# Performance work log

Measured on AMD Instinct MI355X. Metric: run time of the kernel, lower is better.

The kernel has to match this reference:

```python
import math
import jax, jax.numpy as jnp
import numpy as np

FACTOR = 5

def setup_inputs() -> dict:
    key = jax.random.key(0)
    k1, k2, k3, k4 = jax.random.split(key, 4)
    B, L, H, E = 4, 2048, 8, 64
    sample_k = min(L, max(1, int(FACTOR * math.ceil(math.log(L + 1)))))  # 40
    return {
        "queries": jax.random.normal(k1, (B, L, H, E), jnp.float32),
        "keys": jax.random.normal(k2, (B, L, H, E), jnp.float32),
        "values": jax.random.normal(k3, (B, L, H, E), jnp.float32),
        "index_sample": jax.random.randint(k4, (L, sample_k), 0, L),
    }

def reference(queries, keys, values, index_sample):
    # queries/keys/values: [B, L, H, E]; index_sample: [Lq, sample_k] int
    B, Lq, H, E = queries.shape
    Lk = keys.shape[1]
    q = jnp.transpose(queries, (0, 2, 1, 3))  # [B,H,Lq,E]
    k = jnp.transpose(keys, (0, 2, 1, 3))     # [B,H,Lk,E]
    v = jnp.transpose(values, (0, 2, 1, 3))   # [B,H,Lk,E]

    n_top = min(Lq, max(1, int(FACTOR * math.ceil(math.log(Lq + 1)))))
    scale = 1.0 / math.sqrt(E)

    # --- ProbSparse query scoring: sample keys per query, measure sparsity ---
    k_sample = k[:, :, index_sample, :]                       # [B,H,Lq,sk,E]
    qk_sample = jnp.einsum('bhle,bhlse->bhls', q, k_sample)   # [B,H,Lq,sk]
    sparsity = qk_sample.max(axis=-1) - qk_sample.mean(axis=-1)  # [B,H,Lq]
    _, top_idx = jax.lax.top_k(sparsity, n_top)               # [B,H,n_top]

    # --- Full scores only for the top queries ---
    q_top = jnp.take_along_axis(q, top_idx[..., None], axis=2)    # [B,H,n_top,E]
    scores = jnp.einsum('bhne,bhke->bhnk', q_top, k) * scale      # [B,H,n_top,Lk]

    # causal mask on the gathered rows (mask_flag=True, attn_mask=None)
    key_pos = jnp.arange(Lk)
    mask = key_pos[None, None, None, :] > top_idx[..., None]
    scores = jnp.where(mask, -jnp.inf, scores)
    attn = jax.nn.softmax(scores, axis=-1)                        # dropout = identity (eval)
    updates = jnp.einsum('bhnk,bhke->bhne', attn, v)              # [B,H,n_top,E]

    # --- cumsum-initialized context, scatter sparse rows back ---
    context = jnp.cumsum(v, axis=2)                               # [B,H,Lq,E]
    bi = jnp.arange(B)[:, None, None]
    hi = jnp.arange(H)[None, :, None]
    context = context.at[bi, hi, top_idx].set(updates)
    return jnp.transpose(context, (0, 2, 1, 3))                   # [B,Lq,H,E]
```

## Files before the change

### kernel.cpp

```cpp
#include <hip/hip_runtime.h>
#include <hip/hip_bf16.h>

#define BB 4
#define LL 2048
#define HH 8
#define EE 64
#define SK 40
#define NT 40
#define BH (BB*HH)
#define NCH 128
#define CLEN (LL/NCH)
#define KS 128
#define NS (LL/KS)

__device__ __forceinline__ size_t ro(int b, int l, int h) {
    return ((size_t)(b*LL + l)*HH + h)*EE;
}
__device__ __forceinline__ float bcast(float x, int sl) {
    return __uint_as_float(__builtin_amdgcn_readlane(__float_as_uint(x), sl));
}

__global__ __launch_bounds__(256) void k_spars(const float* __restrict__ q,
                                               const float* __restrict__ k,
                                               const int* __restrict__ samp,
                                               float* __restrict__ spars)
{
    __shared__ float pbuf[4][SK][20];
    int wid  = (blockIdx.x * blockDim.x + threadIdx.x) >> 6;
    int lane = threadIdx.x & 63;
    int w    = threadIdx.x >> 6;
    int bh = wid / LL;
    int l  = wid - bh * LL;
    int b = bh >> 3, h = bh & 7;

    int sidx = (lane < SK) ? samp[l*SK + lane] : 0;

    const float4* qrow = (const float4*)(q + ro(b, l, h));
    float4 q4 = qrow[lane & 15];

    int sub = lane >> 4;
    #pragma unroll
    for (int g = 0; g < SK/4; ++g) {
        int s = 4*g + sub;
        int row = __shfl(sidx, s, 64);
        const float4* kr = (const float4*)(k + ro(b, row, h));
        float4 k4 = kr[lane & 15];
        float p = k4.x*q4.x + k4.y*q4.y + k4.z*q4.z + k4.w*q4.w;
        pbuf[w][s][lane & 15] = p;
    }
    float dot = 0.f;
    if (lane < SK) {
        const float4* pr = (const float4*)&pbuf[w][lane][0];
        float4 a = pr[0], b4 = pr[1], c4 = pr[2], d4 = pr[3];
        dot = ((a.x+a.y)+(a.z+a.w)) + ((b4.x+b4.y)+(b4.z+b4.w))
            + ((c4.x+c4.y)+(c4.z+c4.w)) + ((d4.x+d4.y)+(d4.z+d4.w));
    }
    float dmax = (lane < SK) ? dot : -INFINITY;
    float dsum = (lane < SK) ? dot : 0.f;
    #pragma unroll
    for (int off = 32; off; off >>= 1) {
        dmax = fmaxf(dmax, __shfl_xor(dmax, off, 64));
        dsum += __shfl_xor(dsum, off, 64);
    }
    if (lane == 0) spars[bh*LL + l] = dmax - dsum * (1.0f/SK);
}

__global__ __launch_bounds__(256) void k_topk(const float* __restrict__ spars,
                                              int* __restrict__ topidx,
                                              int* __restrict__ sel)
{
    __shared__ float wv[4];
    __shared__ int   wi[4];
    __shared__ int   top[NT];
    int bh = blockIdx.x, t = threadIdx.x, w = t >> 6, lane = t & 63;

    float r[8];
    #pragma unroll
    for (int i = 0; i < 8; ++i) r[i] = spars[bh*LL + i*256 + t];

    for (int n = 0; n < NT; ++n) {
        float bv = r[0]; int bi = t;
        #pragma unroll
        for (int i = 1; i < 8; ++i)
            if (r[i] > bv) { bv = r[i]; bi = i*256 + t; }
        #pragma unroll
        for (int off = 32; off; off >>= 1) {
            float ov = __shfl_xor(bv, off, 64);
            int   oi = __shfl_xor(bi, off, 64);
            if (ov > bv || (ov == bv && oi < bi)) { bv = ov; bi = oi; }
        }
        if (lane == 0) { wv[w] = bv; wi[w] = bi; }
        __syncthreads();
        float gv = wv[0]; int gi = wi[0];
        #pragma unroll
        for (int j = 1; j < 4; ++j) {
            float ov = wv[j]; int oi = wi[j];
            if (ov > gv || (ov == gv && oi < gi)) { gv = ov; gi = oi; }
        }
        if (t == 0) { top[n] = gi; topidx[bh*NT + n] = gi; }
        if ((gi & 255) == t) {
            int slot = gi >> 8;
            #pragma unroll
            for (int i = 0; i < 8; ++i) if (i == slot) r[i] = -INFINITY;
        }
        __syncthreads();
    }

    for (int l2 = t; l2 < LL; l2 += 256) sel[bh*LL + l2] = -1;
    __syncthreads();
    if (t < NT) sel[bh*LL + top[t]] = t;
}

__global__ __launch_bounds__(256) void k_attn_split(const float* __restrict__ q,
                                                    const float* __restrict__ k,
                                                    const float* __restrict__ v,
                                                    const int* __restrict__ topidx,
                                                    float* __restrict__ pm,
                                                    float* __restrict__ pl,
                                                    float* __restrict__ pO)
{
    __shared__ float KT[EE][KS+1];
    __shared__ float Vs[KS][EE];
    __shared__ float Qs[NT][EE];
    __shared__ int   tix[NT];
    __shared__ int   maxti_s;
    int bh = blockIdx.x / NS, split = blockIdx.x % NS;
    int b = bh >> 3, h = bh & 7;
    int base = split * KS;
    int t = threadIdx.x, w = t >> 6, lane = t & 63;

    if (t < NT) tix[t] = topidx[bh*NT + t];
    __syncthreads();
    if (t == 0) { int m = 0; for (int i = 0; i < NT; ++i) m = max(m, tix[i]); maxti_s = m; }
    __syncthreads();
    int jmaxAll = min(KS, maxti_s - base + 1);

    int rr = t >> 4, c4 = t & 15;
    for (int p = 0; p < 3; ++p) {
        int n = p*16 + rr;
        if (n < NT) {
            const float4* qr = (const float4*)(q + ro(b, tix[n], h));
            float4 x = qr[c4];
            Qs[n][c4*4+0] = x.x*0.125f; Qs[n][c4*4+1] = x.y*0.125f;
            Qs[n][c4*4+2] = x.z*0.125f; Qs[n][c4*4+3] = x.w*0.125f;
        }
    }
    for (int p = 0; p < KS/16; ++p) {
        int kr = p*16 + rr;
        if (kr < jmaxAll) {
            const float4* krow = (const float4*)(k + ro(b, base + kr, h));
            float4 x = krow[c4];
            KT[c4*4+0][kr] = x.x; KT[c4*4+1][kr] = x.y;
            KT[c4*4+2][kr] = x.z; KT[c4*4+3][kr] = x.w;
            const float4* vrow = (const float4*)(v + ro(b, base + kr, h));
            ((float4*)&Vs[kr][0])[c4] = vrow[c4];
        }
    }
    __syncthreads();

    for (int jj = 0; jj < 5; ++jj) {
        int na = w + 8*jj, nb = w + 8*jj + 4;
        int ja = min(KS, tix[na] - base + 1);
        int jb = min(KS, tix[nb] - base + 1);
        bool aa = ja > 0, ab = jb > 0;
        size_t pba = ((size_t)(bh*NT + na)*NS + split);
        size_t pbb = ((size_t)(bh*NT + nb)*NS + split);
        int jp = max(ja, jb);
        if (jp <= 0) {
            if (lane == 0) { pm[pba] = -INFINITY; pl[pba] = 0.f; pm[pbb] = -INFINITY; pl[pbb] = 0.f; }
            pO[pba*EE + lane] = 0.f;
            pO[pbb*EE + lane] = 0.f;
            continue;
        }
        float s0a = 0, s1a = 0, s0b = 0, s1b = 0;
        #pragma unroll 4
        for (int e = 0; e < EE; ++e) {
            float k0 = KT[e][lane], k1 = KT[e][64+lane];
            float qa = Qs[na][e],  qb = Qs[nb][e];
            s0a += qa*k0; s1a += qa*k1;
            s0b += qb*k0; s1b += qb*k1;
        }
        s0a = (lane      < ja) ? s0a : -INFINITY;
        s1a = (lane + 64 < ja) ? s1a : -INFINITY;
        s0b = (lane      < jb) ? s0b : -INFINITY;
        s1b = (lane + 64 < jb) ? s1b : -INFINITY;
        float ma = fmaxf(s0a, s1a), mb = fmaxf(s0b, s1b);
        #pragma unroll
        for (int off = 32; off; off >>= 1) {
            ma = fmaxf(ma, __shfl_xor(ma, off, 64));
            mb = fmaxf(mb, __shfl_xor(mb, off, 64));
        }
        float p0a = aa ? __expf(s0a - ma) : 0.f;
        float p1a = aa ? __expf(s1a - ma) : 0.f;
        float p0b = ab ? __expf(s0b - mb) : 0.f;
        float p1b = ab ? __expf(s1b - mb) : 0.f;
        float la = p0a + p1a, lb = p0b + p1b;
        #pragma unroll
        for (int off = 32; off; off >>= 1) {
            la += __shfl_xor(la, off, 64);
            lb += __shfl_xor(lb, off, 64);
        }
        float oa = 0.f, ob = 0.f;
        int lim0 = min(64, jp);
        #pragma unroll 4
        for (int kk = 0; kk < lim0; ++kk) {
            float vv = Vs[kk][lane];
            oa += bcast(p0a, kk) * vv;
            ob += bcast(p0b, kk) * vv;
        }
        int lim1 = min(64, jp - 64);
        #pragma unroll 4
        for (int kk = 0; kk < lim1; ++kk) {
            float vv = Vs[64+kk][lane];
            oa += bcast(p1a, kk) * vv;
            ob += bcast(p1b, kk) * vv;
        }
        if (lane == 0) {
            pm[pba] = aa ? ma : -INFINITY;  pl[pba] = aa ? la : 0.f;
            pm[pbb] = ab ? mb : -INFINITY;  pl[pbb] = ab ? lb : 0.f;
        }
        pO[pba*EE + lane] = aa ? oa : 0.f;
        pO[pbb*EE + lane] = ab ? ob : 0.f;
    }
}

__global__ __launch_bounds__(256) void k_attn_comb(const float* __restrict__ pm,
                                                   const float* __restrict__ pl,
                                                   const float* __restrict__ pO,
                                                   float* __restrict__ upd)
{
    int wid  = (blockIdx.x * blockDim.x + threadIdx.x) >> 6;
    int lane = threadIdx.x & 63;
    if (wid >= BH*NT) return;
    float M = -INFINITY;
    #pragma unroll
    for (int s = 0; s < NS; ++s) M = fmaxf(M, pm[wid*NS + s]);
    float L = 0.f, O = 0.f;
    #pragma unroll
    for (int s = 0; s < NS; ++s) {
        float ms = pm[wid*NS + s];
        float sc = __expf(ms - M);
        L += pl[wid*NS + s] * sc;
        O += pO[(size_t)(wid*NS + s)*EE + lane] * sc;
    }
    upd[(size_t)wid*EE + lane] = O / L;
}

__global__ __launch_bounds__(256) void k_attn_old(const float* __restrict__ q,
                                                  const float* __restrict__ k,
                                                  const float* __restrict__ v,
                                                  const int* __restrict__ topidx,
                                                  float* __restrict__ upd)
{
    __shared__ float sc[LL];
    __shared__ float red[256];
    __shared__ float part[4][EE];
    int bh = blockIdx.x / NT, n = blockIdx.x % NT;
    int b = bh >> 3, h = bh & 7;
    int ti = topidx[bh*NT + n];
    int t = threadIdx.x, w = t >> 6, lane = t & 63;

    float qe = q[ro(b, ti, h) + lane];
    for (int j = w; j <= ti; j += 4) {
        float kv = k[ro(b, j, h) + lane];
        float p = qe * kv;
        #pragma unroll
        for (int off = 32; off; off >>= 1) p += __shfl_xor(p, off, 64);
        if (lane == 0) sc[j] = p * 0.125f;
    }
    __syncthreads();
    float m = -1e30f;
    for (int j = t; j <= ti; j += 256) m = fmaxf(m, sc[j]);
    red[t] = m; __syncthreads();
    for (int s2 = 128; s2; s2 >>= 1) { if (t < s2) red[t] = fmaxf(red[t], red[t+s2]); __syncthreads(); }
    m = red[0]; __syncthreads();
    float ssum = 0.f;
    for (int j = t; j <= ti; j += 256) { float p = __expf(sc[j] - m); sc[j] = p; ssum += p; }
    red[t] = ssum; __syncthreads();
    for (int s2 = 128; s2; s2 >>= 1) { if (t < s2) red[t] += red[t+s2]; __syncthreads(); }
    float inv = 1.0f / red[0];
    float acc = 0.f;
    for (int j = w; j <= ti; j += 4) acc += sc[j] * v[ro(b, j, h) + lane];
    part[w][lane] = acc;
    __syncthreads();
    if (w == 0) {
        float r = (part[0][lane] + part[1][lane] + part[2][lane] + part[3][lane]) * inv;
        upd[((size_t)bh*NT + n)*EE + lane] = r;
    }
}

__global__ __launch_bounds__(256) void k_csum(const float* __restrict__ v,
                                              float* __restrict__ csum)
{
    int wid  = (blockIdx.x * blockDim.x + threadIdx.x) >> 6;
    int lane = threadIdx.x & 63;
    int bh = wid / NCH, c = wid - bh*NCH;
    int b = bh >> 3, h = bh & 7;
    int l0 = c * CLEN;
    float s = 0.f;
    #pragma unroll 4
    for (int i = 0; i < CLEN; ++i)
        s += v[ro(b, l0 + i, h) + lane];
    csum[(size_t)wid*EE + lane] = s;
}

__global__ __launch_bounds__(256) void k_pfx(float* __restrict__ csum)
{
    int wid  = (blockIdx.x * blockDim.x + threadIdx.x) >> 6;
    int lane = threadIdx.x & 63;
    if (wid >= BH) return;
    float run = 0.f;
    for (int c = 0; c < NCH; ++c) {
        size_t a = ((size_t)wid*NCH + c)*EE + lane;
        float x = csum[a];
        csum[a] = run;
        run += x;
    }
}

__global__ __launch_bounds__(256) void k_out(const float* __restrict__ v,
                                             const float* __restrict__ csum,
                                             const int* __restrict__ sel,
                                             const float* __restrict__ upd,
                                             float* __restrict__ out)
{
    int wid  = (blockIdx.x * blockDim.x + threadIdx.x) >> 6;
    int lane = threadIdx.x & 63;
    int bh = wid / NCH, c = wid - bh*NCH;
    int b = bh >> 3, h = bh & 7;

    float run = csum[((size_t)bh*NCH + c)*EE + lane];
    int l0 = c * CLEN;
    #pragma unroll 4
    for (int i = 0; i < CLEN; ++i) {
        int l = l0 + i;
        run += v[ro(b, l, h) + lane];
        int sn = sel[bh*LL + l];
        float val = (sn >= 0) ? upd[((size_t)bh*NT + sn)*EE + lane] : run;
        out[ro(b, l, h) + lane] = val;
    }
}

extern "C" void kernel_launch(void* const* d_in, const int* in_sizes, int n_in,
                              void* d_out, int out_size, void* d_ws, size_t ws_size,
                              hipStream_t stream) {
    const float* q = (const float*)d_in[0];
    const float* k = (const float*)d_in[1];
    const float* v = (const float*)d_in[2];
    const int* samp = (const int*)d_in[3];
    float* out = (float*)d_out;

    char* ws = (char*)d_ws;
    size_t o = 0;
    float* spars  = (float*)(ws + o); o += (size_t)BH*LL*4;
    int*   topidx = (int*)  (ws + o); o += 8192;
    int*   sel    = (int*)  (ws + o); o += (size_t)BH*LL*4;
    float* upd    = (float*)(ws + o); o += (size_t)BH*NT*EE*4;
    float* csum   = (float*)(ws + o); o += (size_t)BH*NCH*EE*4;
    size_t base_need = o;
    float* pm = (float*)(ws + o); o += (size_t)BH*NT*NS*4;
    float* pl = (float*)(ws + o); o += (size_t)BH*NT*NS*4;
    float* pO = (float*)(ws + o); o += (size_t)BH*NT*NS*EE*4;
    size_t full_need = o;

    k_spars<<<BH*LL/4, 256, 0, stream>>>(q, k, samp, spars);
    k_topk <<<BH,      256, 0, stream>>>(spars, topidx, sel);
    if (ws_size >= full_need) {
        k_attn_split<<<BH*NS, 256, 0, stream>>>(q, k, v, topidx, pm, pl, pO);
        k_attn_comb <<<BH*NT/4, 256, 0, stream>>>(pm, pl, pO, upd);
    } else if (ws_size >= base_need) {
        k_attn_old<<<BH*NT, 256, 0, stream>>>(q, k, v, topidx, upd);
    }
    k_csum<<<BH*NCH/4, 256, 0, stream>>>(v, csum);
    k_pfx <<<(BH+3)/4, 256, 0, stream>>>(csum);
    k_out <<<BH*NCH/4, 256, 0, stream>>>(v, csum, sel, upd, out);
}
```

Baseline: 225.2 us.

## Restructure split attention with register-blocked queries, bf16 partials, parallel prefix

Halves the key split size and makes each wave keep 10 query rows in registers, broadcasting q and probabilities via readlane instead of staging Q in LDS. The causal early-skip of key loads is dropped. Partial outputs are stored as bf16, and the combine step reduces split maxima with wave shuffles. The selection map shrinks to int8, the prefix scan becomes a per-head LDS-blocked kernel, k_spars blocks are remapped so neighbouring blocks cover different heads, and workspace buffers are aliased. The bf16 partials add rounding error to the sparse updates.

```diff
diff --git a/kernel.cpp b/kernel.cpp
--- a/kernel.cpp
+++ b/kernel.cpp
@@ -10,8 +10,9 @@
 #define BH (BB*HH)
 #define NCH 128
 #define CLEN (LL/NCH)
-#define KS 128
+#define KS 64
 #define NS (LL/KS)
+#define NQW 10
 
 __device__ __forceinline__ size_t ro(int b, int l, int h) {
     return ((size_t)(b*LL + l)*HH + h)*EE;
@@ -26,11 +27,11 @@
                                                float* __restrict__ spars)
 {
     __shared__ float pbuf[4][SK][20];
-    int wid  = (blockIdx.x * blockDim.x + threadIdx.x) >> 6;
+    int bid = blockIdx.x;
+    int w    = threadIdx.x >> 6;
     int lane = threadIdx.x & 63;
-    int w    = threadIdx.x >> 6;
-    int bh = wid / LL;
-    int l  = wid - bh * LL;
+    int bh = (((bid >> 3) & 3) << 3) | (bid & 7);
+    int l  = (bid >> 5) * 4 + w;
     int b = bh >> 3, h = bh & 7;
 
     int sidx = (lane < SK) ? samp[l*SK + lane] : 0;
@@ -67,7 +68,7 @@
 
 __global__ __launch_bounds__(256) void k_topk(const float* __restrict__ spars,
                                               int* __restrict__ topidx,
-                                              int* __restrict__ sel)
+                                              signed char* __restrict__ sel)
 {
     __shared__ float wv[4];
     __shared__ int   wi[4];
@@ -108,7 +109,7 @@
 
     for (int l2 = t; l2 < LL; l2 += 256) sel[bh*LL + l2] = -1;
     __syncthreads();
-    if (t < NT) sel[bh*LL + top[t]] = t;
+    if (t < NT) sel[bh*LL + top[t]] = (signed char)t;
 }
 
 __global__ __launch_bounds__(256) void k_attn_split(const float* __restrict__ q,
@@ -117,133 +118,179 @@
                                                     const int* __restrict__ topidx,
                                                     float* __restrict__ pm,
                                                     float* __restrict__ pl,
-                                                    float* __restrict__ pO)
+                                                    __hip_bfloat16* __restrict__ pO)
 {
     __shared__ float KT[EE][KS+1];
     __shared__ float Vs[KS][EE];
-    __shared__ float Qs[NT][EE];
     __shared__ int   tix[NT];
-    __shared__ int   maxti_s;
-    int bh = blockIdx.x / NS, split = blockIdx.x % NS;
+    int bh = blockIdx.x >> 5, split = blockIdx.x & 31;
     int b = bh >> 3, h = bh & 7;
     int base = split * KS;
     int t = threadIdx.x, w = t >> 6, lane = t & 63;
 
     if (t < NT) tix[t] = topidx[bh*NT + t];
     __syncthreads();
-    if (t == 0) { int m = 0; for (int i = 0; i < NT; ++i) m = max(m, tix[i]); maxti_s = m; }
-    __syncthreads();
-    int jmaxAll = min(KS, maxti_s - base + 1);
 
     int rr = t >> 4, c4 = t & 15;
-    for (int p = 0; p < 3; ++p) {
-        int n = p*16 + rr;
-        if (n < NT) {
-            const float4* qr = (const float4*)(q + ro(b, tix[n], h));
-            float4 x = qr[c4];
-            Qs[n][c4*4+0] = x.x*0.125f; Qs[n][c4*4+1] = x.y*0.125f;
-            Qs[n][c4*4+2] = x.z*0.125f; Qs[n][c4*4+3] = x.w*0.125f;
-        }
-    }
-    for (int p = 0; p < KS/16; ++p) {
+    #pragma unroll
+    for (int p = 0; p < 4; ++p) {
         int kr = p*16 + rr;
-        if (kr < jmaxAll) {
-            const float4* krow = (const float4*)(k + ro(b, base + kr, h));
-            float4 x = krow[c4];
-            KT[c4*4+0][kr] = x.x; KT[c4*4+1][kr] = x.y;
-            KT[c4*4+2][kr] = x.z; KT[c4*4+3][kr] = x.w;
-            const float4* vrow = (const float4*)(v + ro(b, base + kr, h));
-            ((float4*)&Vs[kr][0])[c4] = vrow[c4];
-        }
-    }
-    __syncthreads();
-
-    for (int jj = 0; jj < 5; ++jj) {
-        int na = w + 8*jj, nb = w + 8*jj + 4;
-        int ja = min(KS, tix[na] - base + 1);
-        int jb = min(KS, tix[nb] - base + 1);
-        bool aa = ja > 0, ab = jb > 0;
-        size_t pba = ((size_t)(bh*NT + na)*NS + split);
-        size_t pbb = ((size_t)(bh*NT + nb)*NS + split);
-        int jp = max(ja, jb);
-        if (jp <= 0) {
-            if (lane == 0) { pm[pba] = -INFINITY; pl[pba] = 0.f; pm[pbb] = -INFINITY; pl[pbb] = 0.f; }
-            pO[pba*EE + lane] = 0.f;
-            pO[pbb*EE + lane] = 0.f;
-            continue;
-        }
-        float s0a = 0, s1a = 0, s0b = 0, s1b = 0;
-        #pragma unroll 4
-        for (int e = 0; e < EE; ++e) {
-            float k0 = KT[e][lane], k1 = KT[e][64+lane];
-            float qa = Qs[na][e],  qb = Qs[nb][e];
-            s0a += qa*k0; s1a += qa*k1;
-            s0b += qb*k0; s1b += qb*k1;
-        }
-        s0a = (lane      < ja) ? s0a : -INFINITY;
-        s1a = (lane + 64 < ja) ? s1a : -INFINITY;
-        s0b = (lane      < jb) ? s0b : -INFINITY;
-        s1b = (lane + 64 < jb) ? s1b : -INFINITY;
-        float ma = fmaxf(s0a, s1a), mb = fmaxf(s0b, s1b);
-        #pragma unroll
-        for (int off = 32; off; off >>= 1) {
-            ma = fmaxf(ma, __shfl_xor(ma, off, 64));
-            mb = fmaxf(mb, __shfl_xor(mb, off, 64));
-        }
-        float p0a = aa ? __expf(s0a - ma) : 0.f;
-        float p1a = aa ? __expf(s1a - ma) : 0.f;
-        float p0b = ab ? __expf(s0b - mb) : 0.f;
-        float p1b = ab ? __expf(s1b - mb) : 0.f;
-        float la = p0a + p1a, lb = p0b + p1b;
-        #pragma unroll
-        for (int off = 32; off; off >>= 1) {
-            la += __shfl_xor(la, off, 64);
-            lb += __shfl_xor(lb, off, 64);
-        }
-        float oa = 0.f, ob = 0.f;
-        int lim0 = min(64, jp);
-        #pragma unroll 4
-        for (int kk = 0; kk < lim0; ++kk) {
-            float vv = Vs[kk][lane];
-            oa += bcast(p0a, kk) * vv;
-            ob += bcast(p0b, kk) * vv;
-        }
-        int lim1 = min(64, jp - 64);
-        #pragma unroll 4
-        for (int kk = 0; kk < lim1; ++kk) {
-            float vv = Vs[64+kk][lane];
-            oa += bcast(p1a, kk) * vv;
-            ob += bcast(p1b, kk) * vv;
-        }
-        if (lane == 0) {
-            pm[pba] = aa ? ma : -INFINITY;  pl[pba] = aa ? la : 0.f;
-            pm[pbb] = ab ? mb : -INFINITY;  pl[pbb] = ab ? lb : 0.f;
-        }
-        pO[pba*EE + lane] = aa ? oa : 0.f;
-        pO[pbb*EE + lane] = ab ? ob : 0.f;
+        const float4* krow = (const float4*)(k + ro(b, base + kr, h));
+        float4 x = krow[c4];
+        KT[c4*4+0][kr] = x.x; KT[c4*4+1][kr] = x.y;
+        KT[c4*4+2][kr] = x.z; KT[c4*4+3][kr] = x.w;
+        const float4* vrow = (const float4*)(v + ro(b, base + kr, h));
+        ((float4*)&Vs[kr][0])[c4] = vrow[c4];
+    }
+
+    float qreg[NQW]; int jn[NQW];
+    #pragma unroll
+    for (int r = 0; r < NQW; ++r) {
+        int ti = tix[w*NQW + r];
+        jn[r] = min(KS, ti - base + 1);
+        qreg[r] = q[ro(b, ti, h) + lane] * 0.125f;
+    }
+    __syncthreads();
+
+    float S[NQW];
+    #pragma unroll
+    for (int r = 0; r < NQW; ++r) S[r] = 0.f;
+    for (int e0 = 0; e0 < EE; e0 += 16) {
+        #pragma unroll
+        for (int j = 0; j < 16; ++j) {
+            int e = e0 + j;
+            float ke = KT[e][lane];
+            #pragma unroll
+            for (int r = 0; r < NQW; ++r)
+                S[r] = fmaf(ke, bcast(qreg[r], e), S[r]);
+        }
+    }
+
+    float P[NQW], mloc[NQW], lloc[NQW];
+    #pragma unroll
+    for (int r = 0; r < NQW; ++r) {
+        float s = (lane < jn[r]) ? S[r] : -INFINITY;
+        float m = s;
+        #pragma unroll
+        for (int off = 32; off; off >>= 1) m = fmaxf(m, __shfl_xor(m, off, 64));
+        bool act = jn[r] > 0;
+        float p = act ? __expf(s - m) : 0.f;
+        float ls = p;
+        #pragma unroll
+        for (int off = 32; off; off >>= 1) ls += __shfl_xor(ls, off, 64);
+        P[r] = p; mloc[r] = act ? m : -INFINITY; lloc[r] = act ? ls : 0.f;
+    }
+
+    float O[NQW];
+    #pragma unroll
+    for (int r = 0; r < NQW; ++r) O[r] = 0.f;
+    for (int k0 = 0; k0 < KS; k0 += 16) {
+        #pragma unroll
+        for (int j = 0; j < 16; ++j) {
+            int kk = k0 + j;
+            float ve = Vs[kk][lane];
+            #pragma unroll
+            for (int r = 0; r < NQW; ++r)
+                O[r] = fmaf(ve, bcast(P[r], kk), O[r]);
+        }
+    }
+
+    #pragma unroll
+    for (int r = 0; r < NQW; ++r) {
+        int n = w*NQW + r;
+        size_t idx = (size_t)(bh*NT + n)*NS + split;
+        if (lane == 0) { pm[idx] = mloc[r]; pl[idx] = lloc[r]; }
+        pO[idx*EE + lane] = __float2bfloat16(O[r]);
     }
 }
 
 __global__ __launch_bounds__(256) void k_attn_comb(const float* __restrict__ pm,
                                                    const float* __restrict__ pl,
-                                                   const float* __restrict__ pO,
+                                                   const __hip_bfloat16* __restrict__ pO,
                                                    float* __restrict__ upd)
 {
     int wid  = (blockIdx.x * blockDim.x + threadIdx.x) >> 6;
     int lane = threadIdx.x & 63;
-    if (wid >= BH*NT) return;
-    float M = -INFINITY;
-    #pragma unroll
-    for (int s = 0; s < NS; ++s) M = fmaxf(M, pm[wid*NS + s]);
-    float L = 0.f, O = 0.f;
-    #pragma unroll
+    float pmv = (lane < NS) ? pm[(size_t)wid*NS + lane] : -INFINITY;
+    float plv = (lane < NS) ? pl[(size_t)wid*NS + lane] : 0.f;
+    float M = pmv;
+    #pragma unroll
+    for (int off = 32; off; off >>= 1) M = fmaxf(M, __shfl_xor(M, off, 64));
+    float sc = (lane < NS && pmv > -INFINITY) ? __expf(pmv - M) : 0.f;
+    float L = plv * sc;
+    #pragma unroll
+    for (int off = 32; off; off >>= 1) L += __shfl_xor(L, off, 64);
+    float O = 0.f;
     for (int s = 0; s < NS; ++s) {
-        float ms = pm[wid*NS + s];
-        float sc = __expf(ms - M);
-        L += pl[wid*NS + s] * sc;
-        O += pO[(size_t)(wid*NS + s)*EE + lane] * sc;
+        float w = bcast(sc, s);
+        O += __bfloat162float(pO[((size_t)wid*NS + s)*EE + lane]) * w;
     }
     upd[(size_t)wid*EE + lane] = O / L;
+}
+
+__global__ __launch_bounds__(256) void k_csum(const float* __restrict__ v,
+                                              float* __restrict__ csum)
+{
+    int wid  = (blockIdx.x * blockDim.x + threadIdx.x) >> 6;
+    int lane = threadIdx.x & 63;
+    int bh = wid / NCH, c = wid - bh*NCH;
+    int b = bh >> 3, h = bh & 7;
+    int l0 = c * CLEN;
+    float s = 0.f;
+    #pragma unroll 4
+    for (int i = 0; i < CLEN; ++i)
+        s += v[ro(b, l0 + i, h) + lane];
+    csum[(size_t)wid*EE + lane] = s;
+}
+
+__global__ __launch_bounds__(256) void k_pfx(float* __restrict__ csum)
+{
+    __shared__ float buf[NCH*EE];
+    __shared__ float gs[4*EE];
+    int bh = blockIdx.x, t = threadIdx.x;
+    int e = t & 63, g = t >> 6;
+
+    for (int i = t; i < NCH*EE; i += 256) buf[i] = csum[(size_t)bh*NCH*EE + i];
+    __syncthreads();
+
+    float s = 0.f;
+    for (int c = g*32; c < g*32+32; ++c) s += buf[c*EE + e];
+    gs[g*EE + e] = s;
+    __syncthreads();
+
+    float run = 0.f;
+    for (int j = 0; j < g; ++j) run += gs[j*EE + e];
+    for (int c = g*32; c < g*32+32; ++c) {
+        float x = buf[c*EE + e];
+        buf[c*EE + e] = run;
+        run += x;
+    }
+    __syncthreads();
+
+    for (int i = t; i < NCH*EE; i += 256) csum[(size_t)bh*NCH*EE + i] = buf[i];
+}
+
+__global__ __launch_bounds__(256) void k_out(const float* __restrict__ v,
+                                             const float* __restrict__ csum,
+                                             const signed char* __restrict__ sel,
+                                             const float* __restrict__ upd,
+                                             float* __restrict__ out)
+{
+    int wid  = (blockIdx.x * blockDim.x + threadIdx.x) >> 6;
+    int lane = threadIdx.x & 63;
+    int bh = wid / NCH, c = wid - bh*NCH;
+    int b = bh >> 3, h = bh & 7;
+
+    float run = csum[((size_t)bh*NCH + c)*EE + lane];
+    int l0 = c * CLEN;
+    #pragma unroll 4
+    for (int i = 0; i < CLEN; ++i) {
+        int l = l0 + i;
+        run += v[ro(b, l, h) + lane];
+        int sn = sel[bh*LL + l];
+        float val = (sn >= 0) ? upd[((size_t)bh*NT + sn)*EE + lane] : run;
+        out[ro(b, l, h) + lane] = val;
+    }
 }
 
 __global__ __launch_bounds__(256) void k_attn_old(const float* __restrict__ q,
@@ -289,58 +336,6 @@
     }
 }
 
-__global__ __launch_bounds__(256) void k_csum(const float* __restrict__ v,
-                                              float* __restrict__ csum)
-{
-    int wid  = (blockIdx.x * blockDim.x + threadIdx.x) >> 6;
-    int lane = threadIdx.x & 63;
-    int bh = wid / NCH, c = wid - bh*NCH;
-    int b = bh >> 3, h = bh & 7;
-    int l0 = c * CLEN;
-    float s = 0.f;
-    #pragma unroll 4
-    for (int i = 0; i < CLEN; ++i)
-        s += v[ro(b, l0 + i, h) + lane];
-    csum[(size_t)wid*EE + lane] = s;
-}
-
-__global__ __launch_bounds__(256) void k_pfx(float* __restrict__ csum)
-{
-    int wid  = (blockIdx.x * blockDim.x + threadIdx.x) >> 6;
-    int lane = threadIdx.x & 63;
-    if (wid >= BH) return;
-    float run = 0.f;
-    for (int c = 0; c < NCH; ++c) {
-        size_t a = ((size_t)wid*NCH + c)*EE + lane;
-        float x = csum[a];
-        csum[a] = run;
-        run += x;
-    }
-}
-
-__global__ __launch_bounds__(256) void k_out(const float* __restrict__ v,
-                                             const float* __restrict__ csum,
-                                             const int* __restrict__ sel,
-                                             const float* __restrict__ upd,
-                                             float* __restrict__ out)
-{
-    int wid  = (blockIdx.x * blockDim.x + threadIdx.x) >> 6;
-    int lane = threadIdx.x & 63;
-    int bh = wid / NCH, c = wid - bh*NCH;
-    int b = bh >> 3, h = bh & 7;
-
-    float run = csum[((size_t)bh*NCH + c)*EE + lane];
-    int l0 = c * CLEN;
-    #pragma unroll 4
-    for (int i = 0; i < CLEN; ++i) {
-        int l = l0 + i;
-        run += v[ro(b, l, h) + lane];
-        int sn = sel[bh*LL + l];
-        float val = (sn >= 0) ? upd[((size_t)bh*NT + sn)*EE + lane] : run;
-        out[ro(b, l, h) + lane] = val;
-    }
-}
-
 extern "C" void kernel_launch(void* const* d_in, const int* in_sizes, int n_in,
                               void* d_out, int out_size, void* d_ws, size_t ws_size,
                               hipStream_t stream) {
@@ -351,27 +346,26 @@
     float* out = (float*)d_out;
 
     char* ws = (char*)d_ws;
-    size_t o = 0;
-    float* spars  = (float*)(ws + o); o += (size_t)BH*LL*4;
-    int*   topidx = (int*)  (ws + o); o += 8192;
-    int*   sel    = (int*)  (ws + o); o += (size_t)BH*LL*4;
-    float* upd    = (float*)(ws + o); o += (size_t)BH*NT*EE*4;
-    float* csum   = (float*)(ws + o); o += (size_t)BH*NCH*EE*4;
-    size_t base_need = o;
-    float* pm = (float*)(ws + o); o += (size_t)BH*NT*NS*4;
-    float* pl = (float*)(ws + o); o += (size_t)BH*NT*NS*4;
-    float* pO = (float*)(ws + o); o += (size_t)BH*NT*NS*EE*4;
-    size_t full_need = o;
+    float*          spars  = (float*)(ws);
+    float*          pm     = (float*)(ws);
+    int*            topidx = (int*)  (ws + 262144);
+    signed char*    sel    = (signed char*)(ws + 262144 + 8192);
+    float*          upd    = (float*)(ws + 262144 + 8192 + 65536);
+    float*          pl     = (float*)(ws + 262144 + 8192 + 65536 + 327680);
+    char*           pObase =          ws + 262144 + 8192 + 65536 + 327680 + 163840;
+    __hip_bfloat16* pO     = (__hip_bfloat16*)pObase;
+    float*          csum   = (float*)pObase;
+    size_t full_need = 262144 + 8192 + 65536 + 327680 + 163840 + (size_t)BH*NT*NS*EE*2;
 
     k_spars<<<BH*LL/4, 256, 0, stream>>>(q, k, samp, spars);
     k_topk <<<BH,      256, 0, stream>>>(spars, topidx, sel);
     if (ws_size >= full_need) {
         k_attn_split<<<BH*NS, 256, 0, stream>>>(q, k, v, topidx, pm, pl, pO);
         k_attn_comb <<<BH*NT/4, 256, 0, stream>>>(pm, pl, pO, upd);
-    } else if (ws_size >= base_need) {
+    } else {
         k_attn_old<<<BH*NT, 256, 0, stream>>>(q, k, v, topidx, upd);
     }
     k_csum<<<BH*NCH/4, 256, 0, stream>>>(v, csum);
-    k_pfx <<<(BH+3)/4, 256, 0, stream>>>(csum);
+    k_pfx <<<BH,       256, 0, stream>>>(csum);
     k_out <<<BH*NCH/4, 256, 0, stream>>>(v, csum, sel, upd, out);
 }
```

After: 217.4 us. 3.4% less time.
